# Optimization experiments

Measured on AMD Instinct MI355X. Metric: run time of the kernel, lower is better.

Reference implementation:

```python
import jax, jax.numpy as jnp
import numpy as np

N_EMBD = 1024
N_HEAD = 16
HEAD_SIZE = N_EMBD // N_HEAD  # 64
ROPE_BASE = 10000.0


def apply_rope(x, pos):
    # x: [B, T, H, D] (torchtune layout), interleaved-pair rotation
    D = x.shape[-1]
    theta = 1.0 / (ROPE_BASE ** (jnp.arange(0, D, 2, dtype=jnp.float32) / D))  # [D/2]
    ang = pos.astype(jnp.float32)[:, None] * theta[None, :]                    # [T, D/2]
    cos = jnp.cos(ang)[None, :, None, :].astype(x.dtype)
    sin = jnp.sin(ang)[None, :, None, :].astype(x.dtype)
    xr = x.reshape(*x.shape[:-1], D // 2, 2)
    x0, x1 = xr[..., 0], xr[..., 1]
    out = jnp.stack([x0 * cos - x1 * sin, x1 * cos + x0 * sin], axis=-1)
    return out.reshape(x.shape)


def setup_inputs() -> dict:
    key = jax.random.key(0)
    k1, k2, k3 = jax.random.split(key, 3)
    B, T = 4, 1000
    x = jax.random.normal(k1, (B, T, N_EMBD), dtype=jnp.float32)
    # causal boolean mask (True = attend), as passed to F.scaled_dot_product_attention
    attn_mask = jnp.tril(jnp.ones((T, T), dtype=bool))[None, None, :, :]
    # Linear weights stored as [in, out] (i.e. torch weight transposed), fan-in scaled
    W_attn = jax.random.normal(k2, (N_EMBD, 3 * N_EMBD), dtype=jnp.float32) * (1.0 / np.sqrt(N_EMBD))
    W_proj = jax.random.normal(k3, (N_EMBD, N_EMBD), dtype=jnp.float32) * (1.0 / np.sqrt(N_EMBD))
    return {"x": x, "attn_mask": attn_mask, "W_attn": W_attn, "W_proj": W_proj}


def reference(x, attn_mask, W_attn, W_proj):
    B, T, C = x.shape
    qkv = x @ W_attn                                   # [B, T, 3C]
    q, k, v = jnp.split(qkv, 3, axis=-1)
    q = q.reshape(B, T, N_HEAD, HEAD_SIZE)
    k = k.reshape(B, T, N_HEAD, HEAD_SIZE)
    v = v.reshape(B, T, N_HEAD, HEAD_SIZE)
    pos = jnp.arange(T)
    q = apply_rope(q, pos)
    k = apply_rope(k, pos)
    # causal SDPA (dropout = 0)
    scale = 1.0 / np.sqrt(HEAD_SIZE)
    scores = jnp.einsum('bqhd,bkhd->bhqk', q, k) * scale   # [B, H, T, T]
    neg = jnp.asarray(jnp.finfo(scores.dtype).min, scores.dtype)
    scores = jnp.where(attn_mask, scores, neg)
    probs = jax.nn.softmax(scores, axis=-1)
    y = jnp.einsum('bhqk,bkhd->bqhd', probs, v)             # [B, T, H, D]
    y = y.reshape(B, T, C)
    return y @ W_proj
```

## Files before the change

kernel.cpp:

```cpp
#include <hip/hip_runtime.h>

typedef unsigned short ushortT;
typedef __attribute__((ext_vector_type(8))) short bf16x8;
typedef __attribute__((ext_vector_type(4))) float f32x4;

#define B_ 4
#define T_ 1000
#define C_ 1024
#define H_ 16
#define D_ 64
#define MP 4096

__device__ __forceinline__ ushortT f2bf(float f) {
    unsigned u = __float_as_uint(f);
    u += 0x7fffu + ((u >> 16) & 1u);
    return (ushortT)(u >> 16);
}
__device__ __forceinline__ float bf2f(ushortT u) {
    return __uint_as_float((unsigned)u << 16);
}
__device__ __forceinline__ float fast_exp2(float x) {
#if __has_builtin(__builtin_amdgcn_exp2f)
    return __builtin_amdgcn_exp2f(x);
#else
    return exp2f(x);
#endif
}

__global__ void cast_x_kernel(const float* __restrict__ x, ushortT* __restrict__ Xb) {
    int idx = blockIdx.x * 256 + threadIdx.x;
    int e = idx * 4;
    if (e >= MP * C_) return;
    int r = e >> 10;
    ushort4 o;
    if (r < B_ * T_) {
        float4 v = *(const float4*)(x + (size_t)e);
        o.x = f2bf(v.x); o.y = f2bf(v.y); o.z = f2bf(v.z); o.w = f2bf(v.w);
    } else {
        o.x = o.y = o.z = o.w = 0;
    }
    *(ushort4*)(Xb + e) = o;
}

__global__ void transpose_w_kernel(const float* __restrict__ W, ushortT* __restrict__ Wt, int N) {
    __shared__ float tile[64][65];
    int k0 = blockIdx.y * 64, n0 = blockIdx.x * 64;
    int lane = threadIdx.x & 63, w4 = threadIdx.x >> 6;
#pragma unroll 4
    for (int i = 0; i < 16; ++i) {
        int row = i * 4 + w4;
        tile[row][lane] = W[(size_t)(k0 + row) * N + n0 + lane];
    }
    __syncthreads();
#pragma unroll 4
    for (int i = 0; i < 16; ++i) {
        int row = i * 4 + w4;
        Wt[(size_t)(n0 + row) * 1024 + k0 + lane] = f2bf(tile[lane][row]);
    }
}

#define BM 128
#define BN 128
#define BK 64

__device__ __forceinline__ void gemm_store(float* p, float v)   { *p = v; }
__device__ __forceinline__ void gemm_store(ushortT* p, float v) { *p = f2bf(v); }

template <typename OutT>
__global__ __launch_bounds__(256, 2) void gemm_bf16_kernel(
    const ushortT* __restrict__ A, const ushortT* __restrict__ Bt,
    OutT* __restrict__ C, int M, int N, int K, int Mstore)
{
    __shared__ ushortT As[BM * BK];
    __shared__ ushortT Bs[BN * BK];
    int tid = threadIdx.x;
    int wave = tid >> 6, lane = tid & 63;
    int m0 = blockIdx.y * BM;
    int n0 = blockIdx.x * BN;
    int wm = (wave >> 1) * 64;
    int wn = (wave & 1) * 64;

    f32x4 acc[4][4] = {};

    int nk = K / BK;
    for (int kt = 0; kt < nk; ++kt) {
        int k0 = kt * BK;
        __syncthreads();
#pragma unroll
        for (int it = 0; it < 4; ++it) {
            int gci = (wave * 4 + it) * 64 + lane;
            int r = gci >> 3;
            int c = gci & 7;
            int sc = c ^ (r & 7);
            const ushortT* ga = A + (size_t)(m0 + r) * K + k0 + sc * 8;
            __builtin_amdgcn_global_load_lds(
                (const __attribute__((address_space(1))) unsigned int*)ga,
                (__attribute__((address_space(3))) unsigned int*)(As + (wave * 4 + it) * 512),
                16, 0, 0);
            const ushortT* gb = Bt + (size_t)(n0 + r) * K + k0 + sc * 8;
            __builtin_amdgcn_global_load_lds(
                (const __attribute__((address_space(1))) unsigned int*)gb,
                (__attribute__((address_space(3))) unsigned int*)(Bs + (wave * 4 + it) * 512),
                16, 0, 0);
        }
        __syncthreads();
        int quad = lane >> 4;
#pragma unroll
        for (int s = 0; s < 2; ++s) {
            int g = s * 4 + quad;
            bf16x8 af[4], bfr[4];
#pragma unroll
            for (int mi = 0; mi < 4; ++mi) {
                int r = wm + mi * 16 + (lane & 15);
                af[mi] = *(const bf16x8*)(As + r * 64 + ((g ^ (r & 7)) * 8));
            }
#pragma unroll
            for (int ni = 0; ni < 4; ++ni) {
                int r = wn + ni * 16 + (lane & 15);
                bfr[ni] = *(const bf16x8*)(Bs + r * 64 + ((g ^ (r & 7)) * 8));
            }
#pragma unroll
            for (int mi = 0; mi < 4; ++mi)
#pragma unroll
                for (int ni = 0; ni < 4; ++ni)
                    acc[mi][ni] = __builtin_amdgcn_mfma_f32_16x16x32_bf16(
                        af[mi], bfr[ni], acc[mi][ni], 0, 0, 0);
        }
    }

    int quad = lane >> 4, col0 = lane & 15;
#pragma unroll
    for (int mi = 0; mi < 4; ++mi) {
#pragma unroll
        for (int j = 0; j < 4; ++j) {
            int row = m0 + wm + mi * 16 + quad * 4 + j;
            if (row < Mstore) {
                OutT* cp = C + (size_t)row * N + n0 + wn;
#pragma unroll
                for (int ni = 0; ni < 4; ++ni)
                    gemm_store(cp + ni * 16 + col0, acc[mi][ni][j]);
            }
        }
    }
}

#define QSCALE 0.18033688011112042f
__global__ void rope_pack_kernel(const ushortT* __restrict__ qkvb,
                                 ushortT* __restrict__ Qb, ushortT* __restrict__ Kb) {
    int idx = blockIdx.x * 256 + threadIdx.x;
    int p = idx & 31;
    int h = (idx >> 5) & 15;
    int t = (idx >> 9) & 1023;
    int b = idx >> 19;
    ushort2 qres = make_ushort2(0, 0), kres = make_ushort2(0, 0);
    if (t < T_) {
        const ushortT* src = qkvb + (size_t)(b * T_ + t) * 3072 + h * 64 + 2 * p;
        ushort2 qu = *(const ushort2*)(src);
        ushort2 ku = *(const ushort2*)(src + 1024);
        float q0 = bf2f(qu.x), q1 = bf2f(qu.y);
        float k0 = bf2f(ku.x), k1 = bf2f(ku.y);
        float theta = __expf(-(float)p * 0.28782313662425572f);
        float ang = (float)t * theta;
        float sn, cs;
        sincosf(ang, &sn, &cs);
        float csq = cs * QSCALE, snq = sn * QSCALE;
        qres = make_ushort2(f2bf(q0 * csq - q1 * snq), f2bf(q1 * csq + q0 * snq));
        kres = make_ushort2(f2bf(k0 * cs - k1 * sn), f2bf(k1 * cs + k0 * sn));
    }
    size_t dst = ((size_t)(b * 16 + h) << 16) + (size_t)t * 64 + 2 * p;
    *(ushort2*)(Qb + dst) = qres;
    *(ushort2*)(Kb + dst) = kres;
}

__global__ void vtrans_kernel(const ushortT* __restrict__ qkvb, ushortT* __restrict__ Vtb) {
    __shared__ __align__(16) ushortT tile[128 * 72];
    int t0 = blockIdx.x * 128;
    int h = blockIdx.y, b = blockIdx.z;
    int tid = threadIdx.x;
#pragma unroll
    for (int it = 0; it < 4; ++it) {
        int cid = it * 256 + tid;
        int r = cid >> 3, c = cid & 7;
        int t = t0 + r;
        bf16x8 v = {};
        if (t < T_) v = *(const bf16x8*)(qkvb + (size_t)(b * T_ + t) * 3072 + 2048 + h * 64 + c * 8);
        *(bf16x8*)(tile + r * 72 + c * 8) = v;
    }
    __syncthreads();
    int bh = b * 16 + h;
#pragma unroll
    for (int it = 0; it < 4; ++it) {
        int u = it * 256 + tid;
        int d = u >> 4, c = u & 15;
        ushortT tmp[8];
#pragma unroll
        for (int j = 0; j < 8; ++j) tmp[j] = tile[(j * 16 + c) * 72 + d];
        *(bf16x8*)(Vtb + ((size_t)bh << 16) + (size_t)d * 1024 + t0 + c * 8) = *(bf16x8*)tmp;
    }
}

#define PSTR 136
template <bool LAST>
__device__ __forceinline__ void softmax_store(f32x4* sc4, ushortT* Ps,
                                              int wave, int quad, int col0,
                                              int q0, int j0) {
#pragma unroll
    for (int reg = 0; reg < 4; ++reg) {
        int m = quad * 4 + reg;
        int q = q0 + wave * 16 + m;
        float pv[8];
#pragma unroll
        for (int nt = 0; nt < 8; ++nt) {
            float p = fast_exp2(sc4[nt][reg]);
            if (LAST && (j0 + nt * 16 + col0) > q) p = 0.f;
            pv[nt] = p;
        }
        int4 pk;
        pk.x = __builtin_amdgcn_perm(__float_as_uint(pv[1]), __float_as_uint(pv[0]), 0x07060302u);
        pk.y = __builtin_amdgcn_perm(__float_as_uint(pv[3]), __float_as_uint(pv[2]), 0x07060302u);
        pk.z = __builtin_amdgcn_perm(__float_as_uint(pv[5]), __float_as_uint(pv[4]), 0x07060302u);
        pk.w = __builtin_amdgcn_perm(__float_as_uint(pv[7]), __float_as_uint(pv[6]), 0x07060302u);
        *(int4*)(Ps + (wave * 16 + m) * PSTR + col0 * 8) = pk;
    }
}

__global__ __launch_bounds__(256, 3) void attn_mfma_kernel(
    const ushortT* __restrict__ Qb, const ushortT* __restrict__ Kb,
    const ushortT* __restrict__ Vtb, ushortT* __restrict__ Yb)
{
    __shared__ __align__(16) ushortT Ks[128 * 64];
    __shared__ __align__(16) ushortT Vs[64 * 128];
    __shared__ __align__(16) ushortT Ps[64 * PSTR];

    int bh = blockIdx.x;
    int b = bh >> 4, h = bh & 15;
    int qi = 15 - blockIdx.y;
    int q0 = qi * 64;
    int tid = threadIdx.x, wave = tid >> 6, lane = tid & 63;
    int col0 = lane & 15, quad = lane >> 4;

    const ushortT* Kbh  = Kb  + ((size_t)bh << 16);
    const ushortT* Vtbh = Vtb + ((size_t)bh << 16);

    const ushortT* qrowp = Qb + ((size_t)bh << 16) + (size_t)(q0 + wave * 16 + col0) * 64;
    bf16x8 aq[2];
    aq[0] = *(const bf16x8*)(qrowp + quad * 8);
    aq[1] = *(const bf16x8*)(qrowp + 32 + quad * 8);

    bf16x8 onesb;
#pragma unroll
    for (int i = 0; i < 8; ++i) onesb[i] = (short)0x3F80;

    f32x4 o[4] = {};
    f32x4 lsum = {};

    int nchunks = qi / 2 + 1;
    for (int cc = 0; cc < nchunks; ++cc) {
        int j0 = cc * 128;
        __syncthreads();
#pragma unroll
        for (int it = 0; it < 4; ++it) {
            int gci = (wave * 4 + it) * 64 + lane;
            {
                int r = gci >> 3, c = gci & 7;
                int sc = c ^ (r & 7);
                const ushortT* gk = Kbh + (size_t)(j0 + r) * 64 + sc * 8;
                __builtin_amdgcn_global_load_lds(
                    (const __attribute__((address_space(1))) unsigned int*)gk,
                    (__attribute__((address_space(3))) unsigned int*)(Ks + (wave * 4 + it) * 512),
                    16, 0, 0);
            }
            {
                int d = gci >> 4, c = gci & 15;
                int sc = c ^ (d & 15);
                const ushortT* gv = Vtbh + (size_t)d * 1024 + j0 + sc * 8;
                __builtin_amdgcn_global_load_lds(
                    (const __attribute__((address_space(1))) unsigned int*)gv,
                    (__attribute__((address_space(3))) unsigned int*)(Vs + (wave * 4 + it) * 512),
                    16, 0, 0);
            }
        }
        __syncthreads();

        f32x4 sc4[8] = {};
#pragma unroll
        for (int s = 0; s < 2; ++s) {
#pragma unroll
            for (int nt = 0; nt < 8; ++nt) {
                int r = nt * 16 + col0;
                bf16x8 bk = *(const bf16x8*)(Ks + r * 64 + (((s * 4 + quad) ^ (col0 & 7)) * 8));
                sc4[nt] = __builtin_amdgcn_mfma_f32_16x16x32_bf16(aq[s], bk, sc4[nt], 0, 0, 0);
            }
        }

        if (cc == nchunks - 1)
            softmax_store<true>(sc4, Ps, wave, quad, col0, q0, j0);
        else
            softmax_store<false>(sc4, Ps, wave, quad, col0, q0, j0);

#pragma unroll
        for (int s = 0; s < 4; ++s) {
            bf16x8 ap = *(const bf16x8*)(Ps + (wave * 16 + col0) * PSTR + s * 32 + quad * 8);
            lsum = __builtin_amdgcn_mfma_f32_16x16x32_bf16(ap, onesb, lsum, 0, 0, 0);
#pragma unroll
            for (int nt = 0; nt < 4; ++nt) {
                int d = nt * 16 + col0;
                bf16x8 bv = *(const bf16x8*)(Vs + d * 128 + (((s * 4 + quad) ^ col0) * 8));
                o[nt] = __builtin_amdgcn_mfma_f32_16x16x32_bf16(ap, bv, o[nt], 0, 0, 0);
            }
        }
    }

#pragma unroll
    for (int reg = 0; reg < 4; ++reg) {
        int q = q0 + wave * 16 + quad * 4 + reg;
        if (q < T_) {
            float inv_l = 1.0f / lsum[reg];
            ushortT* yp = Yb + (size_t)(b * T_ + q) * 1024 + h * 64;
#pragma unroll
            for (int nt = 0; nt < 4; ++nt)
                yp[nt * 16 + col0] = f2bf(o[nt][reg] * inv_l);
        }
    }
}

extern "C" void kernel_launch(void* const* d_in, const int* in_sizes, int n_in,
                              void* d_out, int out_size, void* d_ws, size_t ws_size,
                              hipStream_t stream) {
    const float* x      = (const float*)d_in[0];
    const float* W_attn = (const float*)d_in[2];
    const float* W_proj = (const float*)d_in[3];
    float* out = (float*)d_out;

    uintptr_t w = (uintptr_t)d_ws;
    ushortT* Xb   = (ushortT*)(w);
    ushortT* Wat  = (ushortT*)(w + 8388608);
    ushortT* Wpt  = (ushortT*)(w + 14680064);
    ushortT* qkvb = (ushortT*)(w + 16777216);
    ushortT* Qb   = (ushortT*)(w + 41943040);
    ushortT* Kb   = (ushortT*)(w + 50331648);
    ushortT* Vtb  = (ushortT*)(w + 58720256);
    ushortT* Yb   = (ushortT*)(w + 67108864);

    cast_x_kernel<<<dim3((MP * C_ / 4 + 255) / 256), dim3(256), 0, stream>>>(x, Xb);
    transpose_w_kernel<<<dim3(3072 / 64, 1024 / 64), dim3(256), 0, stream>>>(W_attn, Wat, 3072);
    transpose_w_kernel<<<dim3(1024 / 64, 1024 / 64), dim3(256), 0, stream>>>(W_proj, Wpt, 1024);

    gemm_bf16_kernel<ushortT><<<dim3(3072 / BN, MP / BM), dim3(256), 0, stream>>>(
        Xb, Wat, qkvb, MP, 3072, 1024, MP);

    rope_pack_kernel<<<dim3(B_ * 1024 * H_ * 32 / 256), dim3(256), 0, stream>>>(qkvb, Qb, Kb);
    vtrans_kernel<<<dim3(8, H_, B_), dim3(256), 0, stream>>>(qkvb, Vtb);

    attn_mfma_kernel<<<dim3(64, 16), dim3(256), 0, stream>>>(Qb, Kb, Vtb, Yb);

    gemm_bf16_kernel<float><<<dim3(1024 / BN, MP / BM), dim3(256), 0, stream>>>(
        Yb, Wpt, out, MP, 1024, 1024, B_ * T_);
}
```

Measured before the change: 169.6 us.

## Fuse RoPE and V transpose into QKV GEMM epilogue, merge prep kernels

Merges the x cast and both weight transposes into a single prep launch. RoPE (using a per-block sin/cos table in shared memory) and the V transpose now run in the QKV GEMM epilogue, so the intermediate qkv buffer and two extra kernels go away. Rows are padded per batch to 1024 so each GEMM tile maps to one batch. The projection GEMM uses 64-row tiles to launch more blocks. This saves launches and the qkv round trip through global memory, but adds shared-memory epilogue work and scattered 2-byte stores in the Q/K path.

```diff
diff --git a/kernel.cpp b/kernel.cpp
--- a/kernel.cpp
+++ b/kernel.cpp
@@ -1,23 +1,20 @@
 #include <hip/hip_runtime.h>
 
 typedef unsigned short ushortT;
+typedef unsigned int uintT;
 typedef __attribute__((ext_vector_type(8))) short bf16x8;
 typedef __attribute__((ext_vector_type(4))) float f32x4;
 
 #define B_ 4
 #define T_ 1000
-#define C_ 1024
 #define H_ 16
-#define D_ 64
 #define MP 4096
+#define QSCALE 0.18033688011112042f
 
 __device__ __forceinline__ ushortT f2bf(float f) {
     unsigned u = __float_as_uint(f);
     u += 0x7fffu + ((u >> 16) & 1u);
     return (ushortT)(u >> 16);
-}
-__device__ __forceinline__ float bf2f(ushortT u) {
-    return __uint_as_float((unsigned)u << 16);
 }
 __device__ __forceinline__ float fast_exp2(float x) {
 #if __has_builtin(__builtin_amdgcn_exp2f)
@@ -27,25 +24,29 @@
 #endif
 }
 
-__global__ void cast_x_kernel(const float* __restrict__ x, ushortT* __restrict__ Xb) {
-    int idx = blockIdx.x * 256 + threadIdx.x;
-    int e = idx * 4;
-    if (e >= MP * C_) return;
-    int r = e >> 10;
-    ushort4 o;
-    if (r < B_ * T_) {
-        float4 v = *(const float4*)(x + (size_t)e);
-        o.x = f2bf(v.x); o.y = f2bf(v.y); o.z = f2bf(v.z); o.w = f2bf(v.w);
-    } else {
-        o.x = o.y = o.z = o.w = 0;
-    }
-    *(ushort4*)(Xb + e) = o;
-}
-
-__global__ void transpose_w_kernel(const float* __restrict__ W, ushortT* __restrict__ Wt, int N) {
+__global__ void prep_kernel(const float* __restrict__ x,
+                            const float* __restrict__ Wa, const float* __restrict__ Wp,
+                            ushortT* __restrict__ Xb,
+                            ushortT* __restrict__ Wat, ushortT* __restrict__ Wpt) {
     __shared__ float tile[64][65];
-    int k0 = blockIdx.y * 64, n0 = blockIdx.x * 64;
-    int lane = threadIdx.x & 63, w4 = threadIdx.x >> 6;
+    int bid = blockIdx.x, tid = threadIdx.x;
+    if (bid < 4096) {
+        int e = (bid * 256 + tid) * 4;
+        int r = e >> 10, col = e & 1023;
+        int b = r >> 10, t = r & 1023;
+        ushort4 o = make_ushort4(0, 0, 0, 0);
+        if (t < T_) {
+            float4 v = *(const float4*)(x + (((size_t)(b * T_ + t)) << 10) + col);
+            o.x = f2bf(v.x); o.y = f2bf(v.y); o.z = f2bf(v.z); o.w = f2bf(v.w);
+        }
+        *(ushort4*)(Xb + (size_t)e) = o;
+        return;
+    }
+    const float* W; ushortT* Wt; int N, bx, by;
+    if (bid < 4096 + 768) { W = Wa; Wt = Wat; N = 3072; int id = bid - 4096; bx = id % 48; by = id / 48; }
+    else                  { W = Wp; Wt = Wpt; N = 1024; int id = bid - 4864; bx = id & 15; by = id >> 4; }
+    int k0 = by * 64, n0 = bx * 64;
+    int lane = tid & 63, w4 = tid >> 6;
 #pragma unroll 4
     for (int i = 0; i < 16; ++i) {
         int row = i * 4 + w4;
@@ -59,38 +60,28 @@
     }
 }
 
-#define BM 128
-#define BN 128
-#define BK 64
-
-__device__ __forceinline__ void gemm_store(float* p, float v)   { *p = v; }
-__device__ __forceinline__ void gemm_store(ushortT* p, float v) { *p = f2bf(v); }
-
-template <typename OutT>
-__global__ __launch_bounds__(256, 2) void gemm_bf16_kernel(
+__global__ __launch_bounds__(256, 2) void gemm_qkv_kernel(
     const ushortT* __restrict__ A, const ushortT* __restrict__ Bt,
-    OutT* __restrict__ C, int M, int N, int K, int Mstore)
+    ushortT* __restrict__ Qb, ushortT* __restrict__ Kb, ushortT* __restrict__ Vtb)
 {
-    __shared__ ushortT As[BM * BK];
-    __shared__ ushortT Bs[BN * BK];
-    int tid = threadIdx.x;
-    int wave = tid >> 6, lane = tid & 63;
-    int m0 = blockIdx.y * BM;
-    int n0 = blockIdx.x * BN;
-    int wm = (wave >> 1) * 64;
-    int wn = (wave & 1) * 64;
+    __shared__ __align__(16) ushortT smem[16896];
+    ushortT* As = smem;
+    ushortT* Bs = smem + 8192;
+    const int K = 1024;
+    int tid = threadIdx.x, wave = tid >> 6, lane = tid & 63;
+    int m0 = blockIdx.y * 128, n0 = blockIdx.x * 128;
+    int wm = (wave >> 1) * 64, wn = (wave & 1) * 64;
+    int col0 = lane & 15, quad = lane >> 4;
 
     f32x4 acc[4][4] = {};
 
-    int nk = K / BK;
-    for (int kt = 0; kt < nk; ++kt) {
-        int k0 = kt * BK;
+    for (int kt = 0; kt < 16; ++kt) {
+        int k0 = kt * 64;
         __syncthreads();
 #pragma unroll
         for (int it = 0; it < 4; ++it) {
             int gci = (wave * 4 + it) * 64 + lane;
-            int r = gci >> 3;
-            int c = gci & 7;
+            int r = gci >> 3, c = gci & 7;
             int sc = c ^ (r & 7);
             const ushortT* ga = A + (size_t)(m0 + r) * K + k0 + sc * 8;
             __builtin_amdgcn_global_load_lds(
@@ -104,19 +95,18 @@
                 16, 0, 0);
         }
         __syncthreads();
-        int quad = lane >> 4;
 #pragma unroll
         for (int s = 0; s < 2; ++s) {
             int g = s * 4 + quad;
             bf16x8 af[4], bfr[4];
 #pragma unroll
             for (int mi = 0; mi < 4; ++mi) {
-                int r = wm + mi * 16 + (lane & 15);
+                int r = wm + mi * 16 + col0;
                 af[mi] = *(const bf16x8*)(As + r * 64 + ((g ^ (r & 7)) * 8));
             }
 #pragma unroll
             for (int ni = 0; ni < 4; ++ni) {
-                int r = wn + ni * 16 + (lane & 15);
+                int r = wn + ni * 16 + col0;
                 bfr[ni] = *(const bf16x8*)(Bs + r * 64 + ((g ^ (r & 7)) * 8));
             }
 #pragma unroll
@@ -127,75 +117,73 @@
                         af[mi], bfr[ni], acc[mi][ni], 0, 0, 0);
         }
     }
-
-    int quad = lane >> 4, col0 = lane & 15;
-#pragma unroll
-    for (int mi = 0; mi < 4; ++mi) {
-#pragma unroll
-        for (int j = 0; j < 4; ++j) {
-            int row = m0 + wm + mi * 16 + quad * 4 + j;
-            if (row < Mstore) {
-                OutT* cp = C + (size_t)row * N + n0 + wn;
-#pragma unroll
-                for (int ni = 0; ni < 4; ++ni)
-                    gemm_store(cp + ni * 16 + col0, acc[mi][ni][j]);
-            }
-        }
-    }
-}
-
-#define QSCALE 0.18033688011112042f
-__global__ void rope_pack_kernel(const ushortT* __restrict__ qkvb,
-                                 ushortT* __restrict__ Qb, ushortT* __restrict__ Kb) {
-    int idx = blockIdx.x * 256 + threadIdx.x;
-    int p = idx & 31;
-    int h = (idx >> 5) & 15;
-    int t = (idx >> 9) & 1023;
-    int b = idx >> 19;
-    ushort2 qres = make_ushort2(0, 0), kres = make_ushort2(0, 0);
-    if (t < T_) {
-        const ushortT* src = qkvb + (size_t)(b * T_ + t) * 3072 + h * 64 + 2 * p;
-        ushort2 qu = *(const ushort2*)(src);
-        ushort2 ku = *(const ushort2*)(src + 1024);
-        float q0 = bf2f(qu.x), q1 = bf2f(qu.y);
-        float k0 = bf2f(ku.x), k1 = bf2f(ku.y);
-        float theta = __expf(-(float)p * 0.28782313662425572f);
-        float ang = (float)t * theta;
-        float sn, cs;
-        sincosf(ang, &sn, &cs);
-        float csq = cs * QSCALE, snq = sn * QSCALE;
-        qres = make_ushort2(f2bf(q0 * csq - q1 * snq), f2bf(q1 * csq + q0 * snq));
-        kres = make_ushort2(f2bf(k0 * cs - k1 * sn), f2bf(k1 * cs + k0 * sn));
-    }
-    size_t dst = ((size_t)(b * 16 + h) << 16) + (size_t)t * 64 + 2 * p;
-    *(ushort2*)(Qb + dst) = qres;
-    *(ushort2*)(Kb + dst) = kres;
-}
-
-__global__ void vtrans_kernel(const ushortT* __restrict__ qkvb, ushortT* __restrict__ Vtb) {
-    __shared__ __align__(16) ushortT tile[128 * 72];
-    int t0 = blockIdx.x * 128;
-    int h = blockIdx.y, b = blockIdx.z;
-    int tid = threadIdx.x;
-#pragma unroll
-    for (int it = 0; it < 4; ++it) {
-        int cid = it * 256 + tid;
-        int r = cid >> 3, c = cid & 7;
-        int t = t0 + r;
-        bf16x8 v = {};
-        if (t < T_) v = *(const bf16x8*)(qkvb + (size_t)(b * T_ + t) * 3072 + 2048 + h * 64 + c * 8);
-        *(bf16x8*)(tile + r * 72 + c * 8) = v;
-    }
     __syncthreads();
-    int bh = b * 16 + h;
-#pragma unroll
-    for (int it = 0; it < 4; ++it) {
-        int u = it * 256 + tid;
-        int d = u >> 4, c = u & 15;
-        ushortT tmp[8];
-#pragma unroll
-        for (int j = 0; j < 8; ++j) tmp[j] = tile[(j * 16 + c) * 72 + d];
-        *(bf16x8*)(Vtb + ((size_t)bh << 16) + (size_t)d * 1024 + t0 + c * 8) = *(bf16x8*)tmp;
+
+    int sec = n0 >> 10, cb = n0 & 1023;
+    int b = m0 >> 10, tbase = m0 & 1023;
+
+    if (sec < 2) {
+        float2* tab = (float2*)smem;
+#pragma unroll
+        for (int i = 0; i < 16; ++i) {
+            int task = i * 256 + tid;
+            int tl = task >> 5, p = task & 31;
+            float theta = __expf(-(float)p * 0.28782313662425572f);
+            float ang = (float)(tbase + tl) * theta;
+            float sn, cs;
+            sincosf(ang, &sn, &cs);
+            tab[tl * 33 + p] = make_float2(cs, sn);
+        }
+        __syncthreads();
+        ushortT* Out = sec ? Kb : Qb;
+        float qs = sec ? 1.0f : QSCALE;
+#pragma unroll
+        for (int mi = 0; mi < 4; ++mi) {
+#pragma unroll
+            for (int j = 0; j < 4; ++j) {
+                int tl = wm + mi * 16 + quad * 4 + j;
+                int t = tbase + tl;
+                bool valid = t < T_;
+#pragma unroll
+                for (int nt = 0; nt < 4; ++nt) {
+                    float xv = acc[mi][nt][j];
+                    float xp = __shfl_xor(xv, 1);
+                    int cl = wn + nt * 16 + col0;
+                    int d = cl & 63;
+                    float2 cssn = tab[tl * 33 + (d >> 1)];
+                    float r = (d & 1) ? (xv * cssn.x + xp * cssn.y)
+                                      : (xv * cssn.x - xp * cssn.y);
+                    r *= qs;
+                    if (valid)
+                        Out[((size_t)((b << 4) | ((cb + cl) >> 6)) << 16) + (t << 6) + d] = f2bf(r);
+                }
+            }
+        }
+    } else {
+        ushortT* Ls = smem;
+#pragma unroll
+        for (int mi = 0; mi < 4; ++mi) {
+#pragma unroll
+            for (int nt = 0; nt < 4; ++nt) {
+                int cl = wn + nt * 16 + col0;
+                int rb = wm + mi * 16 + quad * 4;
+                uintT lo = (uintT)f2bf(acc[mi][nt][0]) | ((uintT)f2bf(acc[mi][nt][1]) << 16);
+                uintT hi = (uintT)f2bf(acc[mi][nt][2]) | ((uintT)f2bf(acc[mi][nt][3]) << 16);
+                *(uint2*)(Ls + cl * 132 + rb) = make_uint2(lo, hi);
+            }
+        }
+        __syncthreads();
+#pragma unroll
+        for (int it = 0; it < 8; ++it) {
+            int u = it * 256 + tid;
+            int cl = u >> 4, c = u & 15;
+            int d = cl & 63, h = (cb + cl) >> 6;
+            ushortT tmp[8];
+#pragma unroll
+            for (int j = 0; j < 8; ++j) tmp[j] = Ls[cl * 132 + j * 16 + c];
+            *(bf16x8*)(Vtb + (((size_t)((b << 4) | h)) << 16) + ((size_t)d << 10) + tbase + c * 8)
+                = *(bf16x8*)tmp;
+        }
     }
 }
 
@@ -316,10 +304,89 @@
         int q = q0 + wave * 16 + quad * 4 + reg;
         if (q < T_) {
             float inv_l = 1.0f / lsum[reg];
-            ushortT* yp = Yb + (size_t)(b * T_ + q) * 1024 + h * 64;
+            ushortT* yp = Yb + ((size_t)(b * 1024 + q) << 10) + h * 64;
 #pragma unroll
             for (int nt = 0; nt < 4; ++nt)
                 yp[nt * 16 + col0] = f2bf(o[nt][reg] * inv_l);
+        }
+    }
+}
+
+__global__ __launch_bounds__(256, 3) void gemm_proj_kernel(
+    const ushortT* __restrict__ A, const ushortT* __restrict__ Bt,
+    float* __restrict__ Cout)
+{
+    __shared__ __align__(16) ushortT As[64 * 64];
+    __shared__ __align__(16) ushortT Bs[128 * 64];
+    const int K = 1024;
+    int tid = threadIdx.x, wave = tid >> 6, lane = tid & 63;
+    int m0 = blockIdx.y * 64, n0 = blockIdx.x * 128;
+    int wm = (wave >> 1) * 32, wn = (wave & 1) * 64;
+    int col0 = lane & 15, quad = lane >> 4;
+
+    f32x4 acc[2][4] = {};
+
+    for (int kt = 0; kt < 16; ++kt) {
+        int k0 = kt * 64;
+        __syncthreads();
+#pragma unroll
+        for (int it = 0; it < 2; ++it) {
+            int gci = it * 256 + tid;
+            int r = gci >> 3, c = gci & 7;
+            int sc = c ^ (r & 7);
+            const ushortT* ga = A + (size_t)(m0 + r) * K + k0 + sc * 8;
+            __builtin_amdgcn_global_load_lds(
+                (const __attribute__((address_space(1))) unsigned int*)ga,
+                (__attribute__((address_space(3))) unsigned int*)(As + it * 2048 + wave * 512),
+                16, 0, 0);
+        }
+#pragma unroll
+        for (int it = 0; it < 4; ++it) {
+            int gci = it * 256 + tid;
+            int r = gci >> 3, c = gci & 7;
+            int sc = c ^ (r & 7);
+            const ushortT* gb = Bt + (size_t)(n0 + r) * K + k0 + sc * 8;
+            __builtin_amdgcn_global_load_lds(
+                (const __attribute__((address_space(1))) unsigned int*)gb,
+                (__attribute__((address_space(3))) unsigned int*)(Bs + it * 2048 + wave * 512),
+                16, 0, 0);
+        }
+        __syncthreads();
+#pragma unroll
+        for (int s = 0; s < 2; ++s) {
+            int g = s * 4 + quad;
+            bf16x8 af[2], bfr[4];
+#pragma unroll
+            for (int mi = 0; mi < 2; ++mi) {
+                int r = wm + mi * 16 + col0;
+                af[mi] = *(const bf16x8*)(As + r * 64 + ((g ^ (r & 7)) * 8));
+            }
+#pragma unroll
+            for (int ni = 0; ni < 4; ++ni) {
+                int r = wn + ni * 16 + col0;
+                bfr[ni] = *(const bf16x8*)(Bs + r * 64 + ((g ^ (r & 7)) * 8));
+            }
+#pragma unroll
+            for (int mi = 0; mi < 2; ++mi)
+#pragma unroll
+                for (int ni = 0; ni < 4; ++ni)
+                    acc[mi][ni] = __builtin_amdgcn_mfma_f32_16x16x32_bf16(
+                        af[mi], bfr[ni], acc[mi][ni], 0, 0, 0);
+        }
+    }
+
+#pragma unroll
+    for (int mi = 0; mi < 2; ++mi) {
+#pragma unroll
+        for (int j = 0; j < 4; ++j) {
+            int row = m0 + wm + mi * 16 + quad * 4 + j;
+            int t = row & 1023, b = row >> 10;
+            if (t < T_) {
+                float* cp = Cout + ((size_t)(b * T_ + t) << 10) + n0 + wn;
+#pragma unroll
+                for (int ni = 0; ni < 4; ++ni)
+                    cp[ni * 16 + col0] = acc[mi][ni][j];
+            }
         }
     }
 }
@@ -333,27 +400,19 @@
     float* out = (float*)d_out;
 
     uintptr_t w = (uintptr_t)d_ws;
-    ushortT* Xb   = (ushortT*)(w);
-    ushortT* Wat  = (ushortT*)(w + 8388608);
-    ushortT* Wpt  = (ushortT*)(w + 14680064);
-    ushortT* qkvb = (ushortT*)(w + 16777216);
-    ushortT* Qb   = (ushortT*)(w + 41943040);
-    ushortT* Kb   = (ushortT*)(w + 50331648);
-    ushortT* Vtb  = (ushortT*)(w + 58720256);
-    ushortT* Yb   = (ushortT*)(w + 67108864);
-
-    cast_x_kernel<<<dim3((MP * C_ / 4 + 255) / 256), dim3(256), 0, stream>>>(x, Xb);
-    transpose_w_kernel<<<dim3(3072 / 64, 1024 / 64), dim3(256), 0, stream>>>(W_attn, Wat, 3072);
-    transpose_w_kernel<<<dim3(1024 / 64, 1024 / 64), dim3(256), 0, stream>>>(W_proj, Wpt, 1024);
-
-    gemm_bf16_kernel<ushortT><<<dim3(3072 / BN, MP / BM), dim3(256), 0, stream>>>(
-        Xb, Wat, qkvb, MP, 3072, 1024, MP);
-
-    rope_pack_kernel<<<dim3(B_ * 1024 * H_ * 32 / 256), dim3(256), 0, stream>>>(qkvb, Qb, Kb);
-    vtrans_kernel<<<dim3(8, H_, B_), dim3(256), 0, stream>>>(qkvb, Vtb);
+    ushortT* Xb  = (ushortT*)(w);
+    ushortT* Wat = (ushortT*)(w + 8388608);
+    ushortT* Wpt = (ushortT*)(w + 14680064);
+    ushortT* Qb  = (ushortT*)(w + 16777216);
+    ushortT* Kb  = (ushortT*)(w + 25165824);
+    ushortT* Vtb = (ushortT*)(w + 33554432);
+    ushortT* Yb  = (ushortT*)(w + 41943040);
+
+    prep_kernel<<<dim3(5120), dim3(256), 0, stream>>>(x, W_attn, W_proj, Xb, Wat, Wpt);
+
+    gemm_qkv_kernel<<<dim3(24, 32), dim3(256), 0, stream>>>(Xb, Wat, Qb, Kb, Vtb);
 
     attn_mfma_kernel<<<dim3(64, 16), dim3(256), 0, stream>>>(Qb, Kb, Vtb, Yb);
 
-    gemm_bf16_kernel<float><<<dim3(1024 / BN, MP / BM), dim3(256), 0, stream>>>(
-        Yb, Wpt, out, MP, 1024, 1024, B_ * T_);
-}
+    gemm_proj_kernel<<<dim3(8, 64), dim3(256), 0, stream>>>(Yb, Wpt, out);
+}
```

After: 155.3 us. -8.5%, faster.
